# Optimization experiments

Hardware: AMD Instinct MI355X
Metric: run time of the kernel (lower is better)

The kernel has to match this reference:

```python
import jax, jax.numpy as jnp
import numpy as np

N_NODES = 50000
N_EDGES = 800000
IN_CH = 128
HID = 64
N_CLASSES = 10


def setup_inputs() -> dict:
    key = jax.random.key(0)
    ks = jax.random.split(key, 8)
    x = jax.random.normal(ks[0], (N_NODES, IN_CH), dtype=jnp.float32)
    edge_index = jax.random.randint(ks[1], (2, N_EDGES), 0, N_NODES, dtype=jnp.int64)
    W1 = jax.random.normal(ks[2], (IN_CH, HID), dtype=jnp.float32) * 0.05
    b1 = jnp.zeros((HID,), dtype=jnp.float32)
    W2 = jax.random.normal(ks[3], (HID, HID), dtype=jnp.float32) * 0.05
    b2 = jnp.zeros((HID,), dtype=jnp.float32)
    Wc = jax.random.normal(ks[4], (HID, N_CLASSES), dtype=jnp.float32) * 0.05
    bc = jnp.zeros((N_CLASSES,), dtype=jnp.float32)
    return {"x": x, "edge_index": edge_index, "W1": W1, "b1": b1,
            "W2": W2, "b2": b2, "Wc": Wc, "bc": bc}


def reference(x, edge_index, W1, b1, W2, b2, Wc, bc):
    n = x.shape[0]
    loop = jnp.arange(n, dtype=edge_index.dtype)
    # add self-loops (PyG GCNConv default)
    src = jnp.concatenate([edge_index[0], loop])
    dst = jnp.concatenate([edge_index[1], loop])
    # symmetric normalization D^{-1/2} (A+I) D^{-1/2}
    deg = jax.ops.segment_sum(jnp.ones_like(dst, dtype=x.dtype), dst, num_segments=n)
    dis = jax.lax.rsqrt(jnp.maximum(deg, 1e-12))  # deg >= 1 because of self-loops
    norm = (dis[src] * dis[dst])[:, None]  # [E+N, 1]

    def gcn_conv(h, W, b):
        hw = h @ W                                   # [n, out]
        agg = jax.ops.segment_sum(hw[src] * norm, dst, num_segments=n)
        return agg + b

    h = jax.nn.relu(gcn_conv(x, W1, b1))
    h = jax.nn.relu(gcn_conv(h, W2, b2))
    return h @ Wc + bc
```

## Files before the change

kernel.cpp:

```cpp
#include <hip/hip_runtime.h>
#include <hip/hip_fp16.h>

#define N_NODES 50000
#define N_EDGES 800000
#define IN_CH 128
#define HID 64
#define N_CLASSES 10

#define BSH 8
#define BNODES 256
#define NBKT ((N_NODES + BNODES - 1) / BNODES)
#define EPB 2048
#define GA ((N_EDGES + EPB - 1) / EPB)
#define WIN 40
#define SLOTS 64


__global__ void k_binA(const int* __restrict__ src, const int* __restrict__ dst,
                       unsigned* __restrict__ binned, int* __restrict__ cntAB, int ne) {
    __shared__ int lcur[NBKT];
    const int tid = threadIdx.x;
    const int blk = blockIdx.x;
    const int e0 = blk * EPB;
    const int ecnt = min(EPB, ne - e0);

    for (int i = tid; i < NBKT; i += 256) lcur[i] = 0;
    __syncthreads();
    for (int i = tid; i < ecnt; i += 256) {
        int s = src[e0 + i];
        int d = dst[e0 + i];
        int b = d >> BSH;
        int p = atomicAdd(&lcur[b], 1);
        if (p < WIN)
            binned[((size_t)b * GA + blk) * WIN + p] =
                ((unsigned)s << BSH) | (unsigned)(d & (BNODES - 1));
    }
    __syncthreads();
    for (int b = tid; b < NBKT; b += 256) cntAB[b * GA + blk] = min(lcur[b], WIN);
}


__global__ void k_binB(const unsigned* __restrict__ binned, const int* __restrict__ cntAB,
                       unsigned short* __restrict__ col, int* __restrict__ deg,
                       float* __restrict__ dis, int n) {
    __shared__ unsigned short lcol[BNODES * SLOTS];
    __shared__ int lcur[BNODES];
    const int k = blockIdx.x;
    const int tid = threadIdx.x;
    const int nodeBase = k << BSH;
    const int nloc = min(BNODES, n - nodeBase);

    for (int i = tid; i < BNODES; i += 256) lcur[i] = 0;
    __syncthreads();

    for (int w = tid; w < GA; w += 256) {
        int cnt = cntAB[k * GA + w];
        const unsigned* wp = &binned[((size_t)k * GA + w) * WIN];
        for (int i = 0; i < cnt; ++i) {
            unsigned v = wp[i];
            int dl = (int)(v & (BNODES - 1));
            int p = atomicAdd(&lcur[dl], 1);
            if (p < SLOTS) lcol[dl * SLOTS + p] = (unsigned short)(v >> BSH);
        }
    }
    __syncthreads();

    const uint4* lv = (const uint4*)lcol;
    uint4* gv = (uint4*)(col + (size_t)nodeBase * SLOTS);
    for (int i = tid; i < nloc * 8; i += 256) gv[i] = lv[i];
    for (int i = tid; i < nloc; i += 256) {
        int d2 = min(lcur[i], SLOTS);
        deg[nodeBase + i] = d2;
        dis[nodeBase + i] = rsqrtf((float)(d2 + 1));
    }
}


template <int K, bool FP16IN>
__global__ void k_gemm64(const void* __restrict__ hv_, const float* __restrict__ W,
                         const float* __restrict__ dis, __half* __restrict__ out, int n) {
    __shared__ float xs[32][K];
    const int tid = threadIdx.x;
    const int col = tid & 63;
    const int wv = tid >> 6;
    const int nodeBase = blockIdx.x * 32;

    if (!FP16IN) {
        const float* h = (const float*)hv_;
        const int total4 = 32 * K / 4;
        const float4* hv = (const float4*)(h + (size_t)nodeBase * K);
        float4* xv = (float4*)&xs[0][0];
        if (nodeBase + 32 <= n) {
            for (int i = tid; i < total4; i += 256) xv[i] = hv[i];
        } else {
            for (int i = tid; i < total4; i += 256) {
                int r = (i * 4) / K;
                float4 z = make_float4(0.f, 0.f, 0.f, 0.f);
                xv[i] = (nodeBase + r < n) ? hv[i] : z;
            }
        }
    } else {
        const __half* h = (const __half*)hv_;
        if (nodeBase + 32 <= n) {
            const uint4* hv = (const uint4*)(h + (size_t)nodeBase * K);
            for (int i = tid; i < 32 * K / 8; i += 256) {
                uint4 v = hv[i];
                const __half2* hp = (const __half2*)&v;
                float* dp = &xs[0][0] + i * 8;
                float2 f0 = __half22float2(hp[0]);
                float2 f1 = __half22float2(hp[1]);
                float2 f2 = __half22float2(hp[2]);
                float2 f3 = __half22float2(hp[3]);
                dp[0] = f0.x; dp[1] = f0.y; dp[2] = f1.x; dp[3] = f1.y;
                dp[4] = f2.x; dp[5] = f2.y; dp[6] = f3.x; dp[7] = f3.y;
            }
        } else {
            for (int i = tid; i < 32 * K; i += 256) {
                int r = i / K;
                xs[r][i - r * K] =
                    (nodeBase + r < n) ? (float)h[(size_t)(nodeBase + r) * K + (i - r * K)] : 0.f;
            }
        }
    }
    __syncthreads();

    float a[8];
    #pragma unroll
    for (int i = 0; i < 8; ++i) a[i] = 0.f;
    const int r0 = wv * 8;
    #pragma unroll 2
    for (int k = 0; k < K; k += 4) {
        float w0 = W[(k + 0) * 64 + col];
        float w1 = W[(k + 1) * 64 + col];
        float w2 = W[(k + 2) * 64 + col];
        float w3 = W[(k + 3) * 64 + col];
        #pragma unroll
        for (int i = 0; i < 8; ++i) {
            float4 xk = *(const float4*)&xs[r0 + i][k];
            a[i] += xk.x * w0 + xk.y * w1 + xk.z * w2 + xk.w * w3;
        }
    }
    #pragma unroll
    for (int i = 0; i < 8; ++i) {
        int nd = nodeBase + r0 + i;
        if (nd < n) out[(size_t)nd * 64 + col] = __float2half(a[i] * dis[nd]);
    }
}


template <bool LAST>
__global__ void k_agg(const int* __restrict__ deg, const unsigned short* __restrict__ col,
                      const float* __restrict__ dis, const __half* __restrict__ hwp,
                      const float* __restrict__ bvec, const float* __restrict__ Wc,
                      const float* __restrict__ bc, __half* __restrict__ hout,
                      float* __restrict__ outp, int n) {
    __shared__ float sh2[8][64];
    const int tid = threadIdx.x;
    const int wv = tid >> 6;
    const int lane = tid & 63;
    const int hf = lane >> 5;
    const int c2 = lane & 31;
    const int node = blockIdx.x * 8 + wv * 2 + hf;

    const int m = deg[node];
    const float ddis = dis[node];
    const unsigned short* cp = col + (size_t)node * SLOTS;
    const __half2* hw2 = (const __half2*)hwp;

    float2 sv = __half22float2(hw2[(size_t)node * 32 + c2]);
    float ax0 = sv.x, ay0 = sv.y, ax1 = 0.f, ay1 = 0.f;
    int e = 0;
    for (; e + 8 <= m; e += 8) {
        uint4 cw = *(const uint4*)(cp + e);
        int s0 = (int)(cw.x & 0xffff), s1 = (int)(cw.x >> 16);
        int s2 = (int)(cw.y & 0xffff), s3 = (int)(cw.y >> 16);
        int s4 = (int)(cw.z & 0xffff), s5 = (int)(cw.z >> 16);
        int s6 = (int)(cw.w & 0xffff), s7 = (int)(cw.w >> 16);
        float2 f0 = __half22float2(hw2[(size_t)s0 * 32 + c2]);
        float2 f1 = __half22float2(hw2[(size_t)s1 * 32 + c2]);
        float2 f2 = __half22float2(hw2[(size_t)s2 * 32 + c2]);
        float2 f3 = __half22float2(hw2[(size_t)s3 * 32 + c2]);
        float2 f4 = __half22float2(hw2[(size_t)s4 * 32 + c2]);
        float2 f5 = __half22float2(hw2[(size_t)s5 * 32 + c2]);
        float2 f6 = __half22float2(hw2[(size_t)s6 * 32 + c2]);
        float2 f7 = __half22float2(hw2[(size_t)s7 * 32 + c2]);
        ax0 += f0.x + f2.x; ay0 += f0.y + f2.y;
        ax1 += f1.x + f3.x; ay1 += f1.y + f3.y;
        ax0 += f4.x + f6.x; ay0 += f4.y + f6.y;
        ax1 += f5.x + f7.x; ay1 += f5.y + f7.y;
    }
    for (; e + 4 <= m; e += 4) {
        uint2 cw = *(const uint2*)(cp + e);
        int s0 = (int)(cw.x & 0xffff), s1 = (int)(cw.x >> 16);
        int s2 = (int)(cw.y & 0xffff), s3 = (int)(cw.y >> 16);
        float2 f0 = __half22float2(hw2[(size_t)s0 * 32 + c2]);
        float2 f1 = __half22float2(hw2[(size_t)s1 * 32 + c2]);
        float2 f2 = __half22float2(hw2[(size_t)s2 * 32 + c2]);
        float2 f3 = __half22float2(hw2[(size_t)s3 * 32 + c2]);
        ax0 += f0.x + f2.x; ay0 += f0.y + f2.y;
        ax1 += f1.x + f3.x; ay1 += f1.y + f3.y;
    }
    for (; e < m; ++e) {
        float2 f = __half22float2(hw2[(size_t)cp[e] * 32 + c2]);
        ax0 += f.x; ay0 += f.y;
    }

    float hx = fmaxf((ax0 + ax1) * ddis + bvec[2 * c2 + 0], 0.f);
    float hy = fmaxf((ay0 + ay1) * ddis + bvec[2 * c2 + 1], 0.f);

    if (!LAST) {
        ((__half2*)hout)[(size_t)node * 32 + c2] = __floats2half2_rn(hx, hy);
    } else {
        const int nl = wv * 2 + hf;
        sh2[nl][2 * c2 + 0] = hx;
        sh2[nl][2 * c2 + 1] = hy;
        __syncthreads();
        if (tid < 8 * N_CLASSES) {
            int r = tid / N_CLASSES;
            int cls = tid - r * N_CLASSES;
            int nd = blockIdx.x * 8 + r;
            float a = bc[cls];
            #pragma unroll 8
            for (int k = 0; k < 64; ++k) a += sh2[r][k] * Wc[k * N_CLASSES + cls];
            outp[(size_t)nd * N_CLASSES + cls] = a;
        }
    }
}

extern "C" void kernel_launch(void* const* d_in, const int* in_sizes, int n_in,
                              void* d_out, int out_size, void* d_ws, size_t ws_size,
                              hipStream_t stream) {
    const float* x  = (const float*)d_in[0];
    const int*   ei = (const int*)d_in[1];
    const float* W1 = (const float*)d_in[2];
    const float* b1 = (const float*)d_in[3];
    const float* W2 = (const float*)d_in[4];
    const float* b2 = (const float*)d_in[5];
    const float* Wc = (const float*)d_in[6];
    const float* bc = (const float*)d_in[7];
    float* out = (float*)d_out;

    const int n = N_NODES;
    const int ne = N_EDGES;
    const int* src = ei;
    const int* dst = ei + ne;

    __half*         h1     = (__half*)d_ws;
    __half*         hwp16  = h1 + (size_t)n * 64;
    unsigned short* colu16 = (unsigned short*)(hwp16 + (size_t)n * 64);
    float*          dis    = (float*)(colu16 + (size_t)NBKT * BNODES * SLOTS);
    int*            deg    = (int*)(dis + n);
    unsigned*       binned = (unsigned*)h1;
    int*            cntAB  = (int*)binned + (size_t)NBKT * GA * WIN;

    const int BS = 256;
    const int gW = n / 8;
    const int gG = (n + 31) / 32;

    k_binA<<<GA, BS, 0, stream>>>(src, dst, binned, cntAB, ne);
    k_binB<<<NBKT, BS, 0, stream>>>(binned, cntAB, colu16, deg, dis, n);

    k_gemm64<IN_CH, false><<<gG, BS, 0, stream>>>(x, W1, dis, hwp16, n);
    k_agg<false><<<gW, BS, 0, stream>>>(deg, colu16, dis, hwp16, b1,
                                        nullptr, nullptr, h1, nullptr, n);

    k_gemm64<HID, true><<<gG, BS, 0, stream>>>(h1, W2, dis, hwp16, n);
    k_agg<true><<<gW, BS, 0, stream>>>(deg, colu16, dis, hwp16, b2,
                                       Wc, bc, nullptr, out, n);
}
```

Before: 125.0 us.

## Split hw features into two channel planes and gather them in two barrier-separated passes

The GEMM output is now written as two 32-channel fp16 planes instead of interleaved 64-channel rows. The aggregation kernel becomes a persistent grid of 1024 blocks. Each block first gathers the low plane for its node groups into shared memory, hits a soft grid-wide spin barrier, then gathers the high plane. The aim is to shrink the gather working set per pass so it fits better in L2/MALL. In exchange each lane now does scalar half loads instead of half2, there is a spin barrier with a timeout (no guarantee of co-residency), and shared-memory usage per block rises.

```diff
diff --git a/kernel.cpp b/kernel.cpp
--- a/kernel.cpp
+++ b/kernel.cpp
@@ -14,6 +14,10 @@
 #define GA ((N_EDGES + EPB - 1) / EPB)
 #define WIN 40
 #define SLOTS 64
+
+#define AGG_GRID 1024
+#define NGROUP (N_NODES / 8)
+#define MAXG 7
 
 
 __global__ void k_binA(const int* __restrict__ src, const int* __restrict__ dst,
@@ -140,35 +144,35 @@
             a[i] += xk.x * w0 + xk.y * w1 + xk.z * w2 + xk.w * w3;
         }
     }
+    const int plane = col >> 5;
+    const int cc = col & 31;
     #pragma unroll
     for (int i = 0; i < 8; ++i) {
         int nd = nodeBase + r0 + i;
-        if (nd < n) out[(size_t)nd * 64 + col] = __float2half(a[i] * dis[nd]);
-    }
-}
-
-
-template <bool LAST>
-__global__ void k_agg(const int* __restrict__ deg, const unsigned short* __restrict__ col,
-                      const float* __restrict__ dis, const __half* __restrict__ hwp,
-                      const float* __restrict__ bvec, const float* __restrict__ Wc,
-                      const float* __restrict__ bc, __half* __restrict__ hout,
-                      float* __restrict__ outp, int n) {
-    __shared__ float sh2[8][64];
-    const int tid = threadIdx.x;
-    const int wv = tid >> 6;
-    const int lane = tid & 63;
-    const int hf = lane >> 5;
-    const int c2 = lane & 31;
-    const int node = blockIdx.x * 8 + wv * 2 + hf;
-
-    const int m = deg[node];
-    const float ddis = dis[node];
-    const unsigned short* cp = col + (size_t)node * SLOTS;
-    const __half2* hw2 = (const __half2*)hwp;
-
-    float2 sv = __half22float2(hw2[(size_t)node * 32 + c2]);
-    float ax0 = sv.x, ay0 = sv.y, ax1 = 0.f, ay1 = 0.f;
+        if (nd < n)
+            out[(size_t)plane * N_NODES * 32 + (size_t)nd * 32 + cc] =
+                __float2half(a[i] * dis[nd]);
+    }
+}
+
+
+__device__ __forceinline__ void grid_soft_barrier(int* bar, int nblk) {
+    __syncthreads();
+    if (threadIdx.x == 0) {
+        atomicAdd(bar, 1);
+        int spin = 0;
+        while (__hip_atomic_load(bar, __ATOMIC_RELAXED, __HIP_MEMORY_SCOPE_AGENT) < nblk &&
+               ++spin < 20000) {
+            __builtin_amdgcn_s_sleep(8);
+        }
+    }
+    __syncthreads();
+}
+
+
+__device__ __forceinline__ float gsum(const unsigned short* __restrict__ cp, int m,
+                                      const __half* __restrict__ P, int c) {
+    float a0 = 0.f, a1 = 0.f, a2 = 0.f, a3 = 0.f;
     int e = 0;
     for (; e + 8 <= m; e += 8) {
         uint4 cw = *(const uint4*)(cp + e);
@@ -176,53 +180,95 @@
         int s2 = (int)(cw.y & 0xffff), s3 = (int)(cw.y >> 16);
         int s4 = (int)(cw.z & 0xffff), s5 = (int)(cw.z >> 16);
         int s6 = (int)(cw.w & 0xffff), s7 = (int)(cw.w >> 16);
-        float2 f0 = __half22float2(hw2[(size_t)s0 * 32 + c2]);
-        float2 f1 = __half22float2(hw2[(size_t)s1 * 32 + c2]);
-        float2 f2 = __half22float2(hw2[(size_t)s2 * 32 + c2]);
-        float2 f3 = __half22float2(hw2[(size_t)s3 * 32 + c2]);
-        float2 f4 = __half22float2(hw2[(size_t)s4 * 32 + c2]);
-        float2 f5 = __half22float2(hw2[(size_t)s5 * 32 + c2]);
-        float2 f6 = __half22float2(hw2[(size_t)s6 * 32 + c2]);
-        float2 f7 = __half22float2(hw2[(size_t)s7 * 32 + c2]);
-        ax0 += f0.x + f2.x; ay0 += f0.y + f2.y;
-        ax1 += f1.x + f3.x; ay1 += f1.y + f3.y;
-        ax0 += f4.x + f6.x; ay0 += f4.y + f6.y;
-        ax1 += f5.x + f7.x; ay1 += f5.y + f7.y;
+        float v0 = __half2float(P[(size_t)s0 * 32 + c]);
+        float v1 = __half2float(P[(size_t)s1 * 32 + c]);
+        float v2 = __half2float(P[(size_t)s2 * 32 + c]);
+        float v3 = __half2float(P[(size_t)s3 * 32 + c]);
+        float v4 = __half2float(P[(size_t)s4 * 32 + c]);
+        float v5 = __half2float(P[(size_t)s5 * 32 + c]);
+        float v6 = __half2float(P[(size_t)s6 * 32 + c]);
+        float v7 = __half2float(P[(size_t)s7 * 32 + c]);
+        a0 += v0 + v4;
+        a1 += v1 + v5;
+        a2 += v2 + v6;
+        a3 += v3 + v7;
     }
     for (; e + 4 <= m; e += 4) {
         uint2 cw = *(const uint2*)(cp + e);
         int s0 = (int)(cw.x & 0xffff), s1 = (int)(cw.x >> 16);
         int s2 = (int)(cw.y & 0xffff), s3 = (int)(cw.y >> 16);
-        float2 f0 = __half22float2(hw2[(size_t)s0 * 32 + c2]);
-        float2 f1 = __half22float2(hw2[(size_t)s1 * 32 + c2]);
-        float2 f2 = __half22float2(hw2[(size_t)s2 * 32 + c2]);
-        float2 f3 = __half22float2(hw2[(size_t)s3 * 32 + c2]);
-        ax0 += f0.x + f2.x; ay0 += f0.y + f2.y;
-        ax1 += f1.x + f3.x; ay1 += f1.y + f3.y;
-    }
-    for (; e < m; ++e) {
-        float2 f = __half22float2(hw2[(size_t)cp[e] * 32 + c2]);
-        ax0 += f.x; ay0 += f.y;
-    }
-
-    float hx = fmaxf((ax0 + ax1) * ddis + bvec[2 * c2 + 0], 0.f);
-    float hy = fmaxf((ay0 + ay1) * ddis + bvec[2 * c2 + 1], 0.f);
-
-    if (!LAST) {
-        ((__half2*)hout)[(size_t)node * 32 + c2] = __floats2half2_rn(hx, hy);
-    } else {
-        const int nl = wv * 2 + hf;
-        sh2[nl][2 * c2 + 0] = hx;
-        sh2[nl][2 * c2 + 1] = hy;
-        __syncthreads();
-        if (tid < 8 * N_CLASSES) {
-            int r = tid / N_CLASSES;
-            int cls = tid - r * N_CLASSES;
-            int nd = blockIdx.x * 8 + r;
-            float a = bc[cls];
-            #pragma unroll 8
-            for (int k = 0; k < 64; ++k) a += sh2[r][k] * Wc[k * N_CLASSES + cls];
-            outp[(size_t)nd * N_CLASSES + cls] = a;
+        a0 += __half2float(P[(size_t)s0 * 32 + c]);
+        a1 += __half2float(P[(size_t)s1 * 32 + c]);
+        a2 += __half2float(P[(size_t)s2 * 32 + c]);
+        a3 += __half2float(P[(size_t)s3 * 32 + c]);
+    }
+    for (; e < m; ++e)
+        a0 += __half2float(P[(size_t)cp[e] * 32 + c]);
+    return (a0 + a1) + (a2 + a3);
+}
+
+
+template <bool LAST>
+__global__ __launch_bounds__(256, 4)
+void k_agg(const int* __restrict__ deg, const unsigned short* __restrict__ col,
+           const float* __restrict__ dis, const __half* __restrict__ hwp,
+           const float* __restrict__ bvec, const float* __restrict__ Wc,
+           const float* __restrict__ bc, __half* __restrict__ hout,
+           float* __restrict__ outp, int* __restrict__ bar) {
+    __shared__ float sAcc[MAXG][256];
+    __shared__ float sh2[8][64];
+    const int tid = threadIdx.x;
+    const int wv = tid >> 6;
+    const int lane = tid & 63;
+    const int hf = lane >> 5;
+    const int c = lane & 31;
+
+    {
+        const __half* P = hwp;
+        int gi = 0;
+        for (int g = blockIdx.x; g < NGROUP; g += gridDim.x, ++gi) {
+            const int node = g * 8 + wv * 2 + hf;
+            const int m = deg[node];
+            const unsigned short* cp = col + (size_t)node * SLOTS;
+            float acc = __half2float(P[(size_t)node * 32 + c]);
+            acc += gsum(cp, m, P, c);
+            sAcc[gi][tid] = acc;
+        }
+    }
+
+    grid_soft_barrier(bar, (int)gridDim.x);
+
+    {
+        const __half* P = hwp + (size_t)N_NODES * 32;
+        int gi = 0;
+        for (int g = blockIdx.x; g < NGROUP; g += gridDim.x, ++gi) {
+            const int node = g * 8 + wv * 2 + hf;
+            const int m = deg[node];
+            const unsigned short* cp = col + (size_t)node * SLOTS;
+            float acc = __half2float(P[(size_t)node * 32 + c]);
+            acc += gsum(cp, m, P, c);
+            const float ddis = dis[node];
+            float lo = fmaxf(sAcc[gi][tid] * ddis + bvec[c], 0.f);
+            float hi = fmaxf(acc * ddis + bvec[32 + c], 0.f);
+            if (!LAST) {
+                hout[(size_t)node * 64 + c] = __float2half(lo);
+                hout[(size_t)node * 64 + 32 + c] = __float2half(hi);
+            } else {
+                const int nl = wv * 2 + hf;
+                sh2[nl][c] = lo;
+                sh2[nl][32 + c] = hi;
+                __syncthreads();
+                if (tid < 8 * N_CLASSES) {
+                    int r = tid / N_CLASSES;
+                    int cls = tid - r * N_CLASSES;
+                    int nd = g * 8 + r;
+                    float a = bc[cls];
+                    #pragma unroll 8
+                    for (int k = 0; k < 64; ++k) a += sh2[r][k] * Wc[k * N_CLASSES + cls];
+                    outp[(size_t)nd * N_CLASSES + cls] = a;
+                }
+                __syncthreads();
+            }
         }
     }
 }
@@ -247,24 +293,26 @@
 
     __half*         h1     = (__half*)d_ws;
     __half*         hwp16  = h1 + (size_t)n * 64;
-    unsigned short* colu16 = (unsigned short*)(hwp16 + (size_t)n * 64);
+    unsigned short* colu16 = (unsigned short*)(hwp16 + (size_t)2 * n * 32);
     float*          dis    = (float*)(colu16 + (size_t)NBKT * BNODES * SLOTS);
     int*            deg    = (int*)(dis + n);
+    int*            bar    = deg + n;
     unsigned*       binned = (unsigned*)h1;
     int*            cntAB  = (int*)binned + (size_t)NBKT * GA * WIN;
 
     const int BS = 256;
-    const int gW = n / 8;
     const int gG = (n + 31) / 32;
+
+    hipMemsetAsync(bar, 0, 2 * sizeof(int), stream);
 
     k_binA<<<GA, BS, 0, stream>>>(src, dst, binned, cntAB, ne);
     k_binB<<<NBKT, BS, 0, stream>>>(binned, cntAB, colu16, deg, dis, n);
 
     k_gemm64<IN_CH, false><<<gG, BS, 0, stream>>>(x, W1, dis, hwp16, n);
-    k_agg<false><<<gW, BS, 0, stream>>>(deg, colu16, dis, hwp16, b1,
-                                        nullptr, nullptr, h1, nullptr, n);
+    k_agg<false><<<AGG_GRID, BS, 0, stream>>>(deg, colu16, dis, hwp16, b1,
+                                              nullptr, nullptr, h1, nullptr, bar + 0);
 
     k_gemm64<HID, true><<<gG, BS, 0, stream>>>(h1, W2, dis, hwp16, n);
-    k_agg<true><<<gW, BS, 0, stream>>>(deg, colu16, dis, hwp16, b2,
-                                       Wc, bc, nullptr, out, n);
-}
+    k_agg<true><<<AGG_GRID, BS, 0, stream>>>(deg, colu16, dis, hwp16, b2,
+                                             Wc, bc, nullptr, out, bar + 1);
+}
```

Measured after the change: 304.0 us. 2.43x slower.
